# Kernel tuning notes

Measured on AMD Instinct MI355X. Metric: run time of the kernel, lower is better.

## Reference

```python
import jax, jax.numpy as jnp
import numpy as np

B, L, D, H = 2, 4096, 768, 12
Dh = D // H


def setup_inputs() -> dict:
    key = jax.random.key(0)
    k1, k2, k3 = jax.random.split(key, 3)
    x = jax.random.normal(k1, (B, L, D), dtype=jnp.float32)
    Wqkv = jax.random.normal(k2, (D, 3 * D), dtype=jnp.float32) * 0.02
    bqkv = jnp.zeros((3 * D,), dtype=jnp.float32)
    Wo = jax.random.normal(k3, (D, D), dtype=jnp.float32) * 0.02
    bo = jnp.zeros((D,), dtype=jnp.float32)
    return {"x": x, "Wqkv": Wqkv, "bqkv": bqkv, "Wo": Wo, "bo": bo}


def reference(x, Wqkv, bqkv, Wo, bo):
    Bs, Ls, Ds = x.shape
    # fused QKV projection
    qkv = x @ Wqkv + bqkv  # [B, L, 3D]
    q, k, v = jnp.split(qkv, 3, axis=2)
    q = q.reshape(Bs, Ls, H, Dh)
    k = k.reshape(Bs, Ls, H, Dh)
    v = v.reshape(Bs, Ls, H, Dh)
    # scaled dot-product attention with causal mask (fp32 softmax, as flax dpa with dtype=float32)
    scale = 1.0 / np.sqrt(Dh)
    scores = jnp.einsum('bqhd,bkhd->bhqk', q, k) * scale  # [B, H, L, L]
    causal = jnp.tril(jnp.ones((Ls, Ls), dtype=bool))
    big_neg = jnp.finfo(jnp.float32).min
    scores = jnp.where(causal[None, None, :, :], scores, big_neg)
    attn = jax.nn.softmax(scores, axis=-1)
    y = jnp.einsum('bhqk,bkhd->bqhd', attn, v)  # [B, L, H, Dh]
    y = y.reshape(Bs, Ls, Ds)
    # output projection
    return y @ Wo + bo
```

## Files before the change

kernel.cpp:

```cpp
#include <hip/hip_runtime.h>
#include <hip/hip_bf16.h>
#include <stdint.h>

#define BB 2
#define LL 4096
#define DD 768
#define HH 12
#define DH 64
#define MM (BB * LL)
#define NQKV (3 * DD)
#define KK 768
#define PLANE ((size_t)BB * HH * LL * DH)
#define SQSCALE 0.1803368801111204f

typedef __attribute__((ext_vector_type(8))) short bf16x8;
typedef __attribute__((ext_vector_type(4))) float f32x4;

__device__ __forceinline__ float bf2f(uint16_t u) {
  union { uint32_t u; float f; } c; c.u = ((uint32_t)u) << 16; return c.f;
}
__device__ __forceinline__ uint16_t f2bf(float f) {
  union { float f; uint32_t u; } c; c.f = f;
  return (uint16_t)((c.u + 0x7FFFu + ((c.u >> 16) & 1u)) >> 16);
}
__device__ __forceinline__ uint32_t cvt2(float a, float b) {
  __hip_bfloat162 h = __float22bfloat162_rn(make_float2(a, b));
  union { __hip_bfloat162 h; uint32_t u; } c; c.h = h; return c.u;
}

union H8 { uint16_t h[8]; uint32_t w[4]; uint4 v; };
union B8 { uint2 d[2]; bf16x8 v; };

template <bool F32>
__device__ __forceinline__ H8 load8(const void* p, size_t idx) {
  H8 r;
  if (F32) {
    const float* f = (const float*)p + idx;
    float4 a = *(const float4*)f;
    float4 b = *(const float4*)(f + 4);
    r.w[0] = cvt2(a.x, a.y); r.w[1] = cvt2(a.z, a.w);
    r.w[2] = cvt2(b.x, b.y); r.w[3] = cvt2(b.z, b.w);
  } else {
    r.v = *(const uint4*)((const uint16_t*)p + idx);
  }
  return r;
}

__device__ __forceinline__ void g2l16(const uint16_t* g, uint16_t* l) {
  __builtin_amdgcn_global_load_lds((const __attribute__((address_space(1))) void*)g,
                                   (__attribute__((address_space(3))) void*)l,
                                   16, 0, 0);
}

__global__ void detect_k(const uint16_t* __restrict__ x, int* __restrict__ flag) {
  __shared__ int cnt;
  if (threadIdx.x == 0) cnt = 0;
  __syncthreads();
  int c = 0;
  for (int i = threadIdx.x; i < 4096; i += 256) {
    int e = (x[i] >> 7) & 0xFF;
    if (e == 0xFF || e > 133 || e < 100) c++;
  }
  atomicAdd(&cnt, c);
  __syncthreads();
  if (threadIdx.x == 0) *flag = (cnt > 512) ? 1 : 0;
}

__global__ __launch_bounds__(256) void prep_k(const void* __restrict__ x,
                                              uint16_t* __restrict__ xbf,
                                              const void* __restrict__ Wqkv,
                                              uint16_t* __restrict__ wqkvT,
                                              const void* __restrict__ Wo,
                                              uint16_t* __restrict__ woT,
                                              const int* __restrict__ flag) {
  __shared__ uint16_t Ts[64][65];
  const int fl = *flag;
  const int id = blockIdx.x;
  const int tid = threadIdx.x;
  if (id < 768) {
    size_t base = (size_t)id * 1024 + tid;
#pragma unroll
    for (int j = 0; j < 4; ++j) {
      size_t i = base + j * 256;
      H8 v = fl ? load8<true>(x, i * 8) : load8<false>(x, i * 8);
      *(uint4*)(xbf + i * 8) = v.v;
    }
    return;
  }
  const void* W;
  uint16_t* WT;
  int N, widx;
  if (id < 1200) { W = Wqkv; WT = wqkvT; N = NQKV; widx = id - 768; }
  else           { W = Wo;   WT = woT;   N = DD;   widx = id - 1200; }
  const int nb = N / 64;
  const int n0 = (widx % nb) * 64, k0 = (widx / nb) * 64;
#pragma unroll
  for (int j = 0; j < 16; ++j) {
    int idx = tid + j * 256;
    int r = idx >> 6, c = idx & 63;
    size_t gi = (size_t)(k0 + r) * N + n0 + c;
    float v = fl ? ((const float*)W)[gi] : bf2f(((const uint16_t*)W)[gi]);
    Ts[c][r] = f2bf(v);
  }
  __syncthreads();
#pragma unroll
  for (int j = 0; j < 16; ++j) {
    int idx = tid + j * 256;
    int n = idx >> 6, k = idx & 63;
    WT[(size_t)(n0 + n) * KK + k0 + k] = Ts[n][k];
  }
}

__device__ __forceinline__ void gemm128_core(const uint16_t* __restrict__ A,
                                             const uint16_t* __restrict__ BT,
                                             int m0, int n0,
                                             uint16_t* As, uint16_t* Bs,
                                             f32x4 acc[4][4]) {
  const int tid = threadIdx.x, lane = tid & 63, w = tid >> 6;
  const int quad = lane >> 4, c16 = lane & 15;
  const int wm = w >> 1, wn = w & 1;
  const int srow = lane >> 2, schunk = lane & 3;
  const int rsw = (c16 >> 1) & 3;
  for (int k0 = 0; k0 < KK; k0 += 32) {
#pragma unroll
    for (int i = 0; i < 2; ++i) {
      int row = w * 32 + i * 16 + srow;
      int gch = schunk ^ ((row >> 1) & 3);
      g2l16(A + (size_t)(m0 + row) * KK + k0 + gch * 8, As + (w * 32 + i * 16) * 32);
      g2l16(BT + (size_t)(n0 + row) * KK + k0 + gch * 8, Bs + (w * 32 + i * 16) * 32);
    }
    __syncthreads();
    bf16x8 a[4], b[4];
#pragma unroll
    for (int i = 0; i < 4; ++i) {
      a[i] = *(const bf16x8*)(As + (wm * 64 + i * 16 + c16) * 32 + ((quad ^ rsw) * 8));
      b[i] = *(const bf16x8*)(Bs + (wn * 64 + i * 16 + c16) * 32 + ((quad ^ rsw) * 8));
    }
#pragma unroll
    for (int i = 0; i < 4; ++i)
#pragma unroll
      for (int f = 0; f < 4; ++f)
        acc[i][f] = __builtin_amdgcn_mfma_f32_16x16x32_bf16(a[i], b[f], acc[i][f], 0, 0, 0);
    __syncthreads();
  }
}

__global__ __launch_bounds__(256) void qkv128_k(const uint16_t* __restrict__ X,
                                                const uint16_t* __restrict__ WT,
                                                const void* __restrict__ bias,
                                                uint16_t* __restrict__ planes,
                                                const int* __restrict__ flag) {
  __shared__ __align__(16) uint16_t smem[8704];
  uint16_t* As = smem;
  uint16_t* Bs = smem + 4096;
  const int fl = *flag;
  const int m0 = blockIdx.x * 128, n0 = blockIdx.y * 128;
  f32x4 acc[4][4];
#pragma unroll
  for (int i = 0; i < 4; ++i)
#pragma unroll
    for (int f = 0; f < 4; ++f) acc[i][f] = (f32x4){0.f, 0.f, 0.f, 0.f};
  gemm128_core(X, WT, m0, n0, As, Bs, acc);

  const int tid = threadIdx.x, lane = tid & 63, w = tid >> 6;
  const int quad = lane >> 4, c16 = lane & 15;
  const int wm = w >> 1, wn = w & 1;
  const int which = (n0 >= 2 * DD) ? 2 : (n0 >= DD ? 1 : 0);

  if (which < 2) {
    uint16_t* dst = planes + (size_t)which * PLANE;
    const float sc = (which == 0) ? SQSCALE : 1.0f;
#pragma unroll
    for (int f = 0; f < 4; ++f) {
      int n = n0 + wn * 64 + f * 16 + c16;
      float bv = fl ? ((const float*)bias)[n] : bf2f(((const uint16_t*)bias)[n]);
      int rem = n - which * DD;
      int hh = rem >> 6, dd = rem & 63;
#pragma unroll
      for (int i = 0; i < 4; ++i) {
        uint32_t pa = cvt2((acc[i][f][0] + bv) * sc, (acc[i][f][1] + bv) * sc);
        uint32_t pb = cvt2((acc[i][f][2] + bv) * sc, (acc[i][f][3] + bv) * sc);
        int m = m0 + wm * 64 + i * 16 + quad * 4;
        int b = m >> 12, l = m & (LL - 1);
        uint16_t* base = dst + ((size_t)(b * HH + hh) * LL + l) * DH + dd;
        base[0 * DH] = (uint16_t)pa;
        base[1 * DH] = (uint16_t)(pa >> 16);
        base[2 * DH] = (uint16_t)pb;
        base[3 * DH] = (uint16_t)(pb >> 16);
      }
    }
  } else {
    uint16_t (*Ts)[136] = reinterpret_cast<uint16_t(*)[136]>(smem);
    uint16_t* vtp = planes + 2 * PLANE;
    const int l0 = m0 & (LL - 1), bb = m0 >> 12;
    for (int half = 0; half < 2; ++half) {
      __syncthreads();
      if (wn == half) {
#pragma unroll
        for (int f = 0; f < 4; ++f) {
          int n = n0 + half * 64 + f * 16 + c16;
          float bv = fl ? ((const float*)bias)[n] : bf2f(((const uint16_t*)bias)[n]);
#pragma unroll
          for (int i = 0; i < 4; ++i) {
            uint32_t pa = cvt2(acc[i][f][0] + bv, acc[i][f][1] + bv);
            uint32_t pb = cvt2(acc[i][f][2] + bv, acc[i][f][3] + bv);
            *(uint2*)(&Ts[f * 16 + c16][wm * 64 + i * 16 + quad * 4]) = make_uint2(pa, pb);
          }
        }
      }
      __syncthreads();
#pragma unroll
      for (int j = 0; j < 4; ++j) {
        int idx = tid + j * 256;
        int nl = idx >> 4, ch = idx & 15;
        int rem = n0 + half * 64 + nl - 2 * DD;
        int hh = rem >> 6, dd = rem & 63;
        uint4 val = *(const uint4*)(&Ts[nl][ch * 8]);
        *(uint4*)(vtp + ((size_t)(bb * HH + hh) * DH + dd) * LL + l0 + ch * 8) = val;
      }
    }
  }
}

__global__ __launch_bounds__(256) void attn_k(const uint16_t* __restrict__ planes,
                                              uint16_t* __restrict__ y) {
  __shared__ __align__(16) uint16_t Ks[2][64 * 64];
  __shared__ __align__(16) uint16_t Vt[2][64 * 64];
  __shared__ __align__(16) uint16_t Ps[4][16 * 64];
  const int p = blockIdx.x;
  const int bh = blockIdx.y;
  const uint16_t* qb = planes + (size_t)bh * LL * DH;
  const uint16_t* kb = qb + PLANE;
  const uint16_t* vtb = planes + 2 * PLANE + (size_t)bh * DH * LL;
  const int tid = threadIdx.x, lane = tid & 63, wv = tid >> 6;
  const int quad = lane >> 4, c16 = lane & 15;
  const int r0 = tid >> 3, c0 = tid & 7;
  const int sw0 = r0 & 7;
  const int swf = c16 & 7;
  uint16_t* Psb = Ps[wv];
  const int b = bh / HH, hh = bh - b * HH;
  const int pwbase = c16 * 64;
  const int prd0 = pwbase + (((2 * quad) ^ c16) << 2);
  const int prd1 = pwbase + (((2 * quad + 1) ^ c16) << 2);
  const int prd2 = pwbase + (((8 + 2 * quad) ^ c16) << 2);
  const int prd3 = pwbase + (((8 + 2 * quad + 1) ^ c16) << 2);

  for (int pass = 0; pass < 2; ++pass) {
    const int qi = pass ? p : 63 - p;
    const int q0 = qi * 64;
    const size_t qoff = (size_t)(q0 + wv * 16 + c16) * DH;
    bf16x8 qf0 = *(const bf16x8*)(qb + qoff + quad * 8);
    bf16x8 qf1 = *(const bf16x8*)(qb + qoff + 32 + quad * 8);

    f32x4 o[4];
#pragma unroll
    for (int g = 0; g < 4; ++g) o[g] = (f32x4){0.f, 0.f, 0.f, 0.f};
    float l_i = 0.f;

    uint4 kr0 = *(const uint4*)(kb + (size_t)r0 * DH + c0 * 8);
    uint4 kr1 = *(const uint4*)(kb + (size_t)(r0 + 32) * DH + c0 * 8);
    uint4 vr0 = *(const uint4*)(vtb + (size_t)r0 * LL + c0 * 8);
    uint4 vr1 = *(const uint4*)(vtb + (size_t)(r0 + 32) * LL + c0 * 8);

    for (int t = 0; t <= qi; ++t) {
      uint16_t* kd = Ks[t & 1];
      uint16_t* vd = Vt[t & 1];
      *(uint4*)(kd + r0 * 64 + (c0 ^ sw0) * 8) = kr0;
      *(uint4*)(kd + (r0 + 32) * 64 + (c0 ^ sw0) * 8) = kr1;
      *(uint4*)(vd + r0 * 64 + (c0 ^ sw0) * 8) = vr0;
      *(uint4*)(vd + (r0 + 32) * 64 + (c0 ^ sw0) * 8) = vr1;
      if (t < qi) {
        int t64 = (t + 1) * 64;
        kr0 = *(const uint4*)(kb + (size_t)(t64 + r0) * DH + c0 * 8);
        kr1 = *(const uint4*)(kb + (size_t)(t64 + r0 + 32) * DH + c0 * 8);
        vr0 = *(const uint4*)(vtb + (size_t)r0 * LL + t64 + c0 * 8);
        vr1 = *(const uint4*)(vtb + (size_t)(r0 + 32) * LL + t64 + c0 * 8);
      }
      __syncthreads();

      f32x4 s[4];
#pragma unroll
      for (int f = 0; f < 4; ++f) {
        const uint16_t* krow = kd + (f * 16 + c16) * 64;
        bf16x8 k0f = *(const bf16x8*)(krow + ((quad ^ swf) * 8));
        bf16x8 k1f = *(const bf16x8*)(krow + (((quad + 4) ^ swf) * 8));
        f32x4 z = {0.f, 0.f, 0.f, 0.f};
        z = __builtin_amdgcn_mfma_f32_16x16x32_bf16(k0f, qf0, z, 0, 0, 0);
        z = __builtin_amdgcn_mfma_f32_16x16x32_bf16(k1f, qf1, z, 0, 0, 0);
        s[f] = z;
      }
      const int qg = q0 + wv * 16 + c16;
      if (t == qi) {
#pragma unroll
        for (int f = 0; f < 4; ++f) {
          int key0 = t * 64 + f * 16 + quad * 4;
#pragma unroll
          for (int r = 0; r < 4; ++r) {
            float pv = exp2f(s[f][r]);
            pv = (key0 + r <= qg) ? pv : 0.f;
            s[f][r] = pv;
            l_i += pv;
          }
        }
      } else {
#pragma unroll
        for (int f = 0; f < 4; ++f)
#pragma unroll
          for (int r = 0; r < 4; ++r) {
            float pv = exp2f(s[f][r]);
            s[f][r] = pv;
            l_i += pv;
          }
      }
#pragma unroll
      for (int f = 0; f < 4; ++f) {
        uint32_t w0 = cvt2(s[f][0], s[f][1]);
        uint32_t w1 = cvt2(s[f][2], s[f][3]);
        *(uint2*)(Psb + pwbase + (((f * 4 + quad) ^ c16) << 2)) = make_uint2(w0, w1);
      }
      __asm__ __volatile__("s_waitcnt lgkmcnt(0)" ::: "memory");
      B8 p0, p1;
      p0.d[0] = *(const uint2*)(Psb + prd0);
      p0.d[1] = *(const uint2*)(Psb + prd1);
      p1.d[0] = *(const uint2*)(Psb + prd2);
      p1.d[1] = *(const uint2*)(Psb + prd3);
#pragma unroll
      for (int g = 0; g < 4; ++g) {
        const uint16_t* vrow = vd + (g * 16 + c16) * 64;
        bf16x8 v0 = *(const bf16x8*)(vrow + ((quad ^ swf) * 8));
        bf16x8 v1 = *(const bf16x8*)(vrow + (((quad + 4) ^ swf) * 8));
        o[g] = __builtin_amdgcn_mfma_f32_16x16x32_bf16(p0.v, v0, o[g], 0, 0, 0);
        o[g] = __builtin_amdgcn_mfma_f32_16x16x32_bf16(p1.v, v1, o[g], 0, 0, 0);
      }
    }

    l_i += __shfl_xor(l_i, 16);
    l_i += __shfl_xor(l_i, 32);
    float inv[4];
#pragma unroll
    for (int r = 0; r < 4; ++r)
      inv[r] = 1.f / __shfl(l_i, (quad << 4) + quad * 4 + r);
#pragma unroll
    for (int g = 0; g < 4; ++g) {
      uint32_t pa = cvt2(o[g][0] * inv[0], o[g][1] * inv[1]);
      uint32_t pb = cvt2(o[g][2] * inv[2], o[g][3] * inv[3]);
      int l = q0 + wv * 16 + quad * 4;
      uint16_t* base = y + ((size_t)(b * LL + l)) * DD + hh * DH + g * 16 + c16;
      base[0 * DD] = (uint16_t)pa;
      base[1 * DD] = (uint16_t)(pa >> 16);
      base[2 * DD] = (uint16_t)pb;
      base[3 * DD] = (uint16_t)(pb >> 16);
    }
    __syncthreads();
  }
}

__global__ __launch_bounds__(256) void out64_k(const uint16_t* __restrict__ Y,
                                               const uint16_t* __restrict__ WT,
                                               const void* __restrict__ bias,
                                               void* __restrict__ out,
                                               const int* __restrict__ flag) {
  __shared__ __align__(16) uint16_t As[128 * 32];
  __shared__ __align__(16) uint16_t Bs[64 * 32];
  const int fl = *flag;
  const int m0 = blockIdx.x * 128, n0 = blockIdx.y * 64;
  const int tid = threadIdx.x, lane = tid & 63, w = tid >> 6;
  const int quad = lane >> 4, c16 = lane & 15;
  const int srow = lane >> 2, schunk = lane & 3;
  const int rsw = (c16 >> 1) & 3;
  f32x4 acc[2][4];
#pragma unroll
  for (int i = 0; i < 2; ++i)
#pragma unroll
    for (int f = 0; f < 4; ++f) acc[i][f] = (f32x4){0.f, 0.f, 0.f, 0.f};
  for (int k0 = 0; k0 < KK; k0 += 32) {
#pragma unroll
    for (int i = 0; i < 2; ++i) {
      int row = w * 32 + i * 16 + srow;
      int gch = schunk ^ ((row >> 1) & 3);
      g2l16(Y + (size_t)(m0 + row) * KK + k0 + gch * 8, As + (w * 32 + i * 16) * 32);
    }
    {
      int row = w * 16 + srow;
      int gch = schunk ^ ((row >> 1) & 3);
      g2l16(WT + (size_t)(n0 + row) * KK + k0 + gch * 8, Bs + (w * 16) * 32);
    }
    __syncthreads();
    bf16x8 a[2], bfr[4];
#pragma unroll
    for (int i = 0; i < 2; ++i)
      a[i] = *(const bf16x8*)(As + (w * 32 + i * 16 + c16) * 32 + ((quad ^ rsw) * 8));
#pragma unroll
    for (int f = 0; f < 4; ++f)
      bfr[f] = *(const bf16x8*)(Bs + (f * 16 + c16) * 32 + ((quad ^ rsw) * 8));
#pragma unroll
    for (int i = 0; i < 2; ++i)
#pragma unroll
      for (int f = 0; f < 4; ++f)
        acc[i][f] = __builtin_amdgcn_mfma_f32_16x16x32_bf16(a[i], bfr[f], acc[i][f], 0, 0, 0);
    __syncthreads();
  }
#pragma unroll
  for (int f = 0; f < 4; ++f) {
    int n = n0 + f * 16 + c16;
    float bv = fl ? ((const float*)bias)[n] : bf2f(((const uint16_t*)bias)[n]);
#pragma unroll
    for (int i = 0; i < 2; ++i) {
      int m = m0 + w * 32 + i * 16 + quad * 4;
      if (fl) {
        float* base = (float*)out + (size_t)m * DD + n;
#pragma unroll
        for (int r = 0; r < 4; ++r) base[r * DD] = acc[i][f][r] + bv;
      } else {
        uint32_t pa = cvt2(acc[i][f][0] + bv, acc[i][f][1] + bv);
        uint32_t pb = cvt2(acc[i][f][2] + bv, acc[i][f][3] + bv);
        uint16_t* base = (uint16_t*)out + (size_t)m * DD + n;
        base[0 * DD] = (uint16_t)pa;
        base[1 * DD] = (uint16_t)(pa >> 16);
        base[2 * DD] = (uint16_t)pb;
        base[3 * DD] = (uint16_t)(pb >> 16);
      }
    }
  }
}

extern "C" void kernel_launch(void* const* d_in, const int* in_sizes, int n_in,
                              void* d_out, int out_size, void* d_ws, size_t ws_size,
                              hipStream_t stream) {
  const void* x    = d_in[0];
  const void* Wqkv = d_in[1];
  const void* bqkv = d_in[2];
  const void* Wo   = d_in[3];
  const void* bo   = d_in[4];
  int* flagp = (int*)d_ws;
  uint16_t* planes = (uint16_t*)((char*)d_ws + 64);
  uint16_t* y_ws   = planes + 3 * PLANE;
  uint16_t* wqkvT  = y_ws + (size_t)MM * DD;
  uint16_t* woT    = wqkvT + (size_t)NQKV * KK;
  uint16_t* xbf    = y_ws;

  detect_k<<<1, 256, 0, stream>>>((const uint16_t*)x, flagp);
  prep_k<<<1344, 256, 0, stream>>>(x, xbf, Wqkv, wqkvT, Wo, woT, flagp);
  qkv128_k<<<dim3(MM / 128, NQKV / 128), 256, 0, stream>>>(xbf, wqkvT, bqkv, planes, flagp);
  attn_k<<<dim3(32, BB * HH), 256, 0, stream>>>(planes, y_ws);
  out64_k<<<dim3(MM / 128, DD / 64), 256, 0, stream>>>(y_ws, woT, bo, d_out, flagp);
}
```

Before: 269.3 us.

## Fuse both causal query tiles into one K/V sweep and skip bf16 input copy

The attention kernel used to sweep K/V twice per block, once for the high query tile and once for the low one. It now sweeps once, loading each K/V tile into shared memory a single time and computing both query tiles against it while t <= ql. This halves K/V global loads and barrier count per block, at the cost of more registers for the second accumulator set, which may reduce occupancy. Separately, when the input is already bf16, the QKV GEMM reads x directly and the prep kernel skips the copy into the workspace.

```diff
diff --git a/kernel.cpp b/kernel.cpp
--- a/kernel.cpp
+++ b/kernel.cpp
@@ -78,11 +78,12 @@
   const int id = blockIdx.x;
   const int tid = threadIdx.x;
   if (id < 768) {
+    if (!fl) return;
     size_t base = (size_t)id * 1024 + tid;
 #pragma unroll
     for (int j = 0; j < 4; ++j) {
       size_t i = base + j * 256;
-      H8 v = fl ? load8<true>(x, i * 8) : load8<false>(x, i * 8);
+      H8 v = load8<true>(x, i * 8);
       *(uint4*)(xbf + i * 8) = v.v;
     }
     return;
@@ -145,7 +146,8 @@
   }
 }
 
-__global__ __launch_bounds__(256) void qkv128_k(const uint16_t* __restrict__ X,
+__global__ __launch_bounds__(256) void qkv128_k(const void* __restrict__ xorig,
+                                                const uint16_t* __restrict__ xbf,
                                                 const uint16_t* __restrict__ WT,
                                                 const void* __restrict__ bias,
                                                 uint16_t* __restrict__ planes,
@@ -154,6 +156,7 @@
   uint16_t* As = smem;
   uint16_t* Bs = smem + 4096;
   const int fl = *flag;
+  const uint16_t* X = fl ? xbf : (const uint16_t*)xorig;
   const int m0 = blockIdx.x * 128, n0 = blockIdx.y * 128;
   f32x4 acc[4][4];
 #pragma unroll
@@ -245,61 +248,94 @@
   const int prd2 = pwbase + (((8 + 2 * quad) ^ c16) << 2);
   const int prd3 = pwbase + (((8 + 2 * quad + 1) ^ c16) << 2);
 
-  for (int pass = 0; pass < 2; ++pass) {
-    const int qi = pass ? p : 63 - p;
-    const int q0 = qi * 64;
-    const size_t qoff = (size_t)(q0 + wv * 16 + c16) * DH;
-    bf16x8 qf0 = *(const bf16x8*)(qb + qoff + quad * 8);
-    bf16x8 qf1 = *(const bf16x8*)(qb + qoff + 32 + quad * 8);
-
-    f32x4 o[4];
-#pragma unroll
-    for (int g = 0; g < 4; ++g) o[g] = (f32x4){0.f, 0.f, 0.f, 0.f};
-    float l_i = 0.f;
-
-    uint4 kr0 = *(const uint4*)(kb + (size_t)r0 * DH + c0 * 8);
-    uint4 kr1 = *(const uint4*)(kb + (size_t)(r0 + 32) * DH + c0 * 8);
-    uint4 vr0 = *(const uint4*)(vtb + (size_t)r0 * LL + c0 * 8);
-    uint4 vr1 = *(const uint4*)(vtb + (size_t)(r0 + 32) * LL + c0 * 8);
-
-    for (int t = 0; t <= qi; ++t) {
-      uint16_t* kd = Ks[t & 1];
-      uint16_t* vd = Vt[t & 1];
-      *(uint4*)(kd + r0 * 64 + (c0 ^ sw0) * 8) = kr0;
-      *(uint4*)(kd + (r0 + 32) * 64 + (c0 ^ sw0) * 8) = kr1;
-      *(uint4*)(vd + r0 * 64 + (c0 ^ sw0) * 8) = vr0;
-      *(uint4*)(vd + (r0 + 32) * 64 + (c0 ^ sw0) * 8) = vr1;
-      if (t < qi) {
-        int t64 = (t + 1) * 64;
-        kr0 = *(const uint4*)(kb + (size_t)(t64 + r0) * DH + c0 * 8);
-        kr1 = *(const uint4*)(kb + (size_t)(t64 + r0 + 32) * DH + c0 * 8);
-        vr0 = *(const uint4*)(vtb + (size_t)r0 * LL + t64 + c0 * 8);
-        vr1 = *(const uint4*)(vtb + (size_t)(r0 + 32) * LL + t64 + c0 * 8);
-      }
-      __syncthreads();
-
-      f32x4 s[4];
+  const int qh = 63 - p, ql = p;
+  const size_t qoh = (size_t)(qh * 64 + wv * 16 + c16) * DH;
+  const size_t qol = (size_t)(ql * 64 + wv * 16 + c16) * DH;
+  bf16x8 qh0 = *(const bf16x8*)(qb + qoh + quad * 8);
+  bf16x8 qh1 = *(const bf16x8*)(qb + qoh + 32 + quad * 8);
+  bf16x8 ql0 = *(const bf16x8*)(qb + qol + quad * 8);
+  bf16x8 ql1 = *(const bf16x8*)(qb + qol + 32 + quad * 8);
+
+  f32x4 oh[4], ol[4];
+#pragma unroll
+  for (int g = 0; g < 4; ++g) { oh[g] = (f32x4){0.f,0.f,0.f,0.f}; ol[g] = (f32x4){0.f,0.f,0.f,0.f}; }
+  float lh = 0.f, llo = 0.f;
+
+  uint4 kr0 = *(const uint4*)(kb + (size_t)r0 * DH + c0 * 8);
+  uint4 kr1 = *(const uint4*)(kb + (size_t)(r0 + 32) * DH + c0 * 8);
+  uint4 vr0 = *(const uint4*)(vtb + (size_t)r0 * LL + c0 * 8);
+  uint4 vr1 = *(const uint4*)(vtb + (size_t)(r0 + 32) * LL + c0 * 8);
+
+  const int qgh = qh * 64 + wv * 16 + c16;
+  const int qgl = ql * 64 + wv * 16 + c16;
+
+  for (int t = 0; t <= qh; ++t) {
+    uint16_t* kd = Ks[t & 1];
+    uint16_t* vd = Vt[t & 1];
+    *(uint4*)(kd + r0 * 64 + (c0 ^ sw0) * 8) = kr0;
+    *(uint4*)(kd + (r0 + 32) * 64 + (c0 ^ sw0) * 8) = kr1;
+    *(uint4*)(vd + r0 * 64 + (c0 ^ sw0) * 8) = vr0;
+    *(uint4*)(vd + (r0 + 32) * 64 + (c0 ^ sw0) * 8) = vr1;
+    if (t < qh) {
+      int t64 = (t + 1) * 64;
+      kr0 = *(const uint4*)(kb + (size_t)(t64 + r0) * DH + c0 * 8);
+      kr1 = *(const uint4*)(kb + (size_t)(t64 + r0 + 32) * DH + c0 * 8);
+      vr0 = *(const uint4*)(vtb + (size_t)r0 * LL + t64 + c0 * 8);
+      vr1 = *(const uint4*)(vtb + (size_t)(r0 + 32) * LL + t64 + c0 * 8);
+    }
+    __syncthreads();
+
+    const bool dolo = (t <= ql);
+    f32x4 sh[4], sl[4];
+#pragma unroll
+    for (int f = 0; f < 4; ++f) {
+      const uint16_t* krow = kd + (f * 16 + c16) * 64;
+      bf16x8 k0f = *(const bf16x8*)(krow + ((quad ^ swf) * 8));
+      bf16x8 k1f = *(const bf16x8*)(krow + (((quad + 4) ^ swf) * 8));
+      f32x4 z = {0.f, 0.f, 0.f, 0.f};
+      z = __builtin_amdgcn_mfma_f32_16x16x32_bf16(k0f, qh0, z, 0, 0, 0);
+      z = __builtin_amdgcn_mfma_f32_16x16x32_bf16(k1f, qh1, z, 0, 0, 0);
+      sh[f] = z;
+      if (dolo) {
+        f32x4 zl = {0.f, 0.f, 0.f, 0.f};
+        zl = __builtin_amdgcn_mfma_f32_16x16x32_bf16(k0f, ql0, zl, 0, 0, 0);
+        zl = __builtin_amdgcn_mfma_f32_16x16x32_bf16(k1f, ql1, zl, 0, 0, 0);
+        sl[f] = zl;
+      }
+    }
+    if (t == qh) {
 #pragma unroll
       for (int f = 0; f < 4; ++f) {
-        const uint16_t* krow = kd + (f * 16 + c16) * 64;
-        bf16x8 k0f = *(const bf16x8*)(krow + ((quad ^ swf) * 8));
-        bf16x8 k1f = *(const bf16x8*)(krow + (((quad + 4) ^ swf) * 8));
-        f32x4 z = {0.f, 0.f, 0.f, 0.f};
-        z = __builtin_amdgcn_mfma_f32_16x16x32_bf16(k0f, qf0, z, 0, 0, 0);
-        z = __builtin_amdgcn_mfma_f32_16x16x32_bf16(k1f, qf1, z, 0, 0, 0);
-        s[f] = z;
-      }
-      const int qg = q0 + wv * 16 + c16;
-      if (t == qi) {
+        int key0 = t * 64 + f * 16 + quad * 4;
+#pragma unroll
+        for (int r = 0; r < 4; ++r) {
+          float pv = exp2f(sh[f][r]);
+          pv = (key0 + r <= qgh) ? pv : 0.f;
+          sh[f][r] = pv;
+          lh += pv;
+        }
+      }
+    } else {
+#pragma unroll
+      for (int f = 0; f < 4; ++f)
+#pragma unroll
+        for (int r = 0; r < 4; ++r) {
+          float pv = exp2f(sh[f][r]);
+          sh[f][r] = pv;
+          lh += pv;
+        }
+    }
+    if (dolo) {
+      if (t == ql) {
 #pragma unroll
         for (int f = 0; f < 4; ++f) {
           int key0 = t * 64 + f * 16 + quad * 4;
 #pragma unroll
           for (int r = 0; r < 4; ++r) {
-            float pv = exp2f(s[f][r]);
-            pv = (key0 + r <= qg) ? pv : 0.f;
-            s[f][r] = pv;
-            l_i += pv;
+            float pv = exp2f(sl[f][r]);
+            pv = (key0 + r <= qgl) ? pv : 0.f;
+            sl[f][r] = pv;
+            llo += pv;
           }
         }
       } else {
@@ -307,33 +343,56 @@
         for (int f = 0; f < 4; ++f)
 #pragma unroll
           for (int r = 0; r < 4; ++r) {
-            float pv = exp2f(s[f][r]);
-            s[f][r] = pv;
-            l_i += pv;
+            float pv = exp2f(sl[f][r]);
+            sl[f][r] = pv;
+            llo += pv;
           }
       }
+    }
+#pragma unroll
+    for (int f = 0; f < 4; ++f) {
+      uint32_t w0 = cvt2(sh[f][0], sh[f][1]);
+      uint32_t w1 = cvt2(sh[f][2], sh[f][3]);
+      *(uint2*)(Psb + pwbase + (((f * 4 + quad) ^ c16) << 2)) = make_uint2(w0, w1);
+    }
+    __asm__ __volatile__("s_waitcnt lgkmcnt(0)" ::: "memory");
+    B8 ph0, ph1;
+    ph0.d[0] = *(const uint2*)(Psb + prd0);
+    ph0.d[1] = *(const uint2*)(Psb + prd1);
+    ph1.d[0] = *(const uint2*)(Psb + prd2);
+    ph1.d[1] = *(const uint2*)(Psb + prd3);
+    B8 pl0, pl1;
+    if (dolo) {
 #pragma unroll
       for (int f = 0; f < 4; ++f) {
-        uint32_t w0 = cvt2(s[f][0], s[f][1]);
-        uint32_t w1 = cvt2(s[f][2], s[f][3]);
+        uint32_t w0 = cvt2(sl[f][0], sl[f][1]);
+        uint32_t w1 = cvt2(sl[f][2], sl[f][3]);
         *(uint2*)(Psb + pwbase + (((f * 4 + quad) ^ c16) << 2)) = make_uint2(w0, w1);
       }
       __asm__ __volatile__("s_waitcnt lgkmcnt(0)" ::: "memory");
-      B8 p0, p1;
-      p0.d[0] = *(const uint2*)(Psb + prd0);
-      p0.d[1] = *(const uint2*)(Psb + prd1);
-      p1.d[0] = *(const uint2*)(Psb + prd2);
-      p1.d[1] = *(const uint2*)(Psb + prd3);
-#pragma unroll
-      for (int g = 0; g < 4; ++g) {
-        const uint16_t* vrow = vd + (g * 16 + c16) * 64;
-        bf16x8 v0 = *(const bf16x8*)(vrow + ((quad ^ swf) * 8));
-        bf16x8 v1 = *(const bf16x8*)(vrow + (((quad + 4) ^ swf) * 8));
-        o[g] = __builtin_amdgcn_mfma_f32_16x16x32_bf16(p0.v, v0, o[g], 0, 0, 0);
-        o[g] = __builtin_amdgcn_mfma_f32_16x16x32_bf16(p1.v, v1, o[g], 0, 0, 0);
-      }
-    }
-
+      pl0.d[0] = *(const uint2*)(Psb + prd0);
+      pl0.d[1] = *(const uint2*)(Psb + prd1);
+      pl1.d[0] = *(const uint2*)(Psb + prd2);
+      pl1.d[1] = *(const uint2*)(Psb + prd3);
+    }
+#pragma unroll
+    for (int g = 0; g < 4; ++g) {
+      const uint16_t* vrow = vd + (g * 16 + c16) * 64;
+      bf16x8 v0 = *(const bf16x8*)(vrow + ((quad ^ swf) * 8));
+      bf16x8 v1 = *(const bf16x8*)(vrow + (((quad + 4) ^ swf) * 8));
+      oh[g] = __builtin_amdgcn_mfma_f32_16x16x32_bf16(ph0.v, v0, oh[g], 0, 0, 0);
+      oh[g] = __builtin_amdgcn_mfma_f32_16x16x32_bf16(ph1.v, v1, oh[g], 0, 0, 0);
+      if (dolo) {
+        ol[g] = __builtin_amdgcn_mfma_f32_16x16x32_bf16(pl0.v, v0, ol[g], 0, 0, 0);
+        ol[g] = __builtin_amdgcn_mfma_f32_16x16x32_bf16(pl1.v, v1, ol[g], 0, 0, 0);
+      }
+    }
+  }
+
+#pragma unroll
+  for (int side = 0; side < 2; ++side) {
+    float l_i = side ? llo : lh;
+    const int q0 = (side ? ql : qh) * 64;
     l_i += __shfl_xor(l_i, 16);
     l_i += __shfl_xor(l_i, 32);
     float inv[4];
@@ -342,8 +401,9 @@
       inv[r] = 1.f / __shfl(l_i, (quad << 4) + quad * 4 + r);
 #pragma unroll
     for (int g = 0; g < 4; ++g) {
-      uint32_t pa = cvt2(o[g][0] * inv[0], o[g][1] * inv[1]);
-      uint32_t pb = cvt2(o[g][2] * inv[2], o[g][3] * inv[3]);
+      f32x4 og = side ? ol[g] : oh[g];
+      uint32_t pa = cvt2(og[0] * inv[0], og[1] * inv[1]);
+      uint32_t pb = cvt2(og[2] * inv[2], og[3] * inv[3]);
       int l = q0 + wv * 16 + quad * 4;
       uint16_t* base = y + ((size_t)(b * LL + l)) * DD + hh * DH + g * 16 + c16;
       base[0 * DD] = (uint16_t)pa;
@@ -351,7 +411,6 @@
       base[2 * DD] = (uint16_t)pb;
       base[3 * DD] = (uint16_t)(pb >> 16);
     }
-    __syncthreads();
   }
 }
 
@@ -441,7 +500,7 @@
 
   detect_k<<<1, 256, 0, stream>>>((const uint16_t*)x, flagp);
   prep_k<<<1344, 256, 0, stream>>>(x, xbf, Wqkv, wqkvT, Wo, woT, flagp);
-  qkv128_k<<<dim3(MM / 128, NQKV / 128), 256, 0, stream>>>(xbf, wqkvT, bqkv, planes, flagp);
+  qkv128_k<<<dim3(MM / 128, NQKV / 128), 256, 0, stream>>>(x, xbf, wqkvT, bqkv, planes, flagp);
   attn_k<<<dim3(32, BB * HH), 256, 0, stream>>>(planes, y_ws);
   out64_k<<<dim3(MM / 128, DD / 64), 256, 0, stream>>>(y_ws, woT, bo, d_out, flagp);
 }
```

Result: slower. 305.2 us (+13.4%).

## Double GEMM K-tile to 64 with 8-chunk swizzle and skip bf16 x copy

Applied to the files above, without the earlier changes.

The QKV and output-projection GEMMs now stage 64-wide K slices in LDS instead of 32. The XOR swizzle is widened to 8 chunks, which halves the number of loop iterations and barrier pairs per tile. Separately, when the input is already bf16, the prep kernel no longer copies x into a workspace buffer, and the QKV GEMM reads the original input directly. The cost is twice the LDS per block, which may lower occupancy.

```diff
diff --git a/kernel.cpp b/kernel.cpp
--- a/kernel.cpp
+++ b/kernel.cpp
@@ -78,11 +78,12 @@
   const int id = blockIdx.x;
   const int tid = threadIdx.x;
   if (id < 768) {
+    if (!fl) return;
     size_t base = (size_t)id * 1024 + tid;
 #pragma unroll
     for (int j = 0; j < 4; ++j) {
       size_t i = base + j * 256;
-      H8 v = fl ? load8<true>(x, i * 8) : load8<false>(x, i * 8);
+      H8 v = load8<true>(x, i * 8);
       *(uint4*)(xbf + i * 8) = v.v;
     }
     return;
@@ -119,41 +120,47 @@
   const int tid = threadIdx.x, lane = tid & 63, w = tid >> 6;
   const int quad = lane >> 4, c16 = lane & 15;
   const int wm = w >> 1, wn = w & 1;
-  const int srow = lane >> 2, schunk = lane & 3;
-  const int rsw = (c16 >> 1) & 3;
-  for (int k0 = 0; k0 < KK; k0 += 32) {
-#pragma unroll
-    for (int i = 0; i < 2; ++i) {
-      int row = w * 32 + i * 16 + srow;
-      int gch = schunk ^ ((row >> 1) & 3);
-      g2l16(A + (size_t)(m0 + row) * KK + k0 + gch * 8, As + (w * 32 + i * 16) * 32);
-      g2l16(BT + (size_t)(n0 + row) * KK + k0 + gch * 8, Bs + (w * 32 + i * 16) * 32);
+  const int srow = lane >> 3, schunk = lane & 7;
+  const int rsw = c16 & 7;
+  for (int k0 = 0; k0 < KK; k0 += 64) {
+#pragma unroll
+    for (int j = 0; j < 4; ++j) {
+      int row = w * 32 + j * 8 + srow;
+      int gch = schunk ^ (row & 7);
+      g2l16(A + (size_t)(m0 + row) * KK + k0 + gch * 8, As + (w * 32 + j * 8) * 64);
+      g2l16(BT + (size_t)(n0 + row) * KK + k0 + gch * 8, Bs + (w * 32 + j * 8) * 64);
     }
     __syncthreads();
-    bf16x8 a[4], b[4];
-#pragma unroll
-    for (int i = 0; i < 4; ++i) {
-      a[i] = *(const bf16x8*)(As + (wm * 64 + i * 16 + c16) * 32 + ((quad ^ rsw) * 8));
-      b[i] = *(const bf16x8*)(Bs + (wn * 64 + i * 16 + c16) * 32 + ((quad ^ rsw) * 8));
-    }
-#pragma unroll
-    for (int i = 0; i < 4; ++i)
-#pragma unroll
-      for (int f = 0; f < 4; ++f)
-        acc[i][f] = __builtin_amdgcn_mfma_f32_16x16x32_bf16(a[i], b[f], acc[i][f], 0, 0, 0);
+#pragma unroll
+    for (int h = 0; h < 2; ++h) {
+      bf16x8 a[4], b[4];
+      const int ch = ((h * 4 + quad) ^ rsw) * 8;
+#pragma unroll
+      for (int i = 0; i < 4; ++i) {
+        a[i] = *(const bf16x8*)(As + (wm * 64 + i * 16 + c16) * 64 + ch);
+        b[i] = *(const bf16x8*)(Bs + (wn * 64 + i * 16 + c16) * 64 + ch);
+      }
+#pragma unroll
+      for (int i = 0; i < 4; ++i)
+#pragma unroll
+        for (int f = 0; f < 4; ++f)
+          acc[i][f] = __builtin_amdgcn_mfma_f32_16x16x32_bf16(a[i], b[f], acc[i][f], 0, 0, 0);
+    }
     __syncthreads();
   }
 }
 
-__global__ __launch_bounds__(256) void qkv128_k(const uint16_t* __restrict__ X,
+__global__ __launch_bounds__(256) void qkv128_k(const void* __restrict__ xorig,
+                                                const uint16_t* __restrict__ xbf,
                                                 const uint16_t* __restrict__ WT,
                                                 const void* __restrict__ bias,
                                                 uint16_t* __restrict__ planes,
                                                 const int* __restrict__ flag) {
-  __shared__ __align__(16) uint16_t smem[8704];
+  __shared__ __align__(16) uint16_t smem[16384];
   uint16_t* As = smem;
-  uint16_t* Bs = smem + 4096;
+  uint16_t* Bs = smem + 8192;
   const int fl = *flag;
+  const uint16_t* X = fl ? xbf : (const uint16_t*)xorig;
   const int m0 = blockIdx.x * 128, n0 = blockIdx.y * 128;
   f32x4 acc[4][4];
 #pragma unroll
@@ -360,44 +367,49 @@
                                                const void* __restrict__ bias,
                                                void* __restrict__ out,
                                                const int* __restrict__ flag) {
-  __shared__ __align__(16) uint16_t As[128 * 32];
-  __shared__ __align__(16) uint16_t Bs[64 * 32];
+  __shared__ __align__(16) uint16_t As[128 * 64];
+  __shared__ __align__(16) uint16_t Bs[64 * 64];
   const int fl = *flag;
   const int m0 = blockIdx.x * 128, n0 = blockIdx.y * 64;
   const int tid = threadIdx.x, lane = tid & 63, w = tid >> 6;
   const int quad = lane >> 4, c16 = lane & 15;
-  const int srow = lane >> 2, schunk = lane & 3;
-  const int rsw = (c16 >> 1) & 3;
+  const int srow = lane >> 3, schunk = lane & 7;
+  const int rsw = c16 & 7;
   f32x4 acc[2][4];
 #pragma unroll
   for (int i = 0; i < 2; ++i)
 #pragma unroll
     for (int f = 0; f < 4; ++f) acc[i][f] = (f32x4){0.f, 0.f, 0.f, 0.f};
-  for (int k0 = 0; k0 < KK; k0 += 32) {
-#pragma unroll
-    for (int i = 0; i < 2; ++i) {
-      int row = w * 32 + i * 16 + srow;
-      int gch = schunk ^ ((row >> 1) & 3);
-      g2l16(Y + (size_t)(m0 + row) * KK + k0 + gch * 8, As + (w * 32 + i * 16) * 32);
-    }
-    {
-      int row = w * 16 + srow;
-      int gch = schunk ^ ((row >> 1) & 3);
-      g2l16(WT + (size_t)(n0 + row) * KK + k0 + gch * 8, Bs + (w * 16) * 32);
+  for (int k0 = 0; k0 < KK; k0 += 64) {
+#pragma unroll
+    for (int j = 0; j < 4; ++j) {
+      int row = w * 32 + j * 8 + srow;
+      int gch = schunk ^ (row & 7);
+      g2l16(Y + (size_t)(m0 + row) * KK + k0 + gch * 8, As + (w * 32 + j * 8) * 64);
+    }
+#pragma unroll
+    for (int j = 0; j < 2; ++j) {
+      int row = w * 16 + j * 8 + srow;
+      int gch = schunk ^ (row & 7);
+      g2l16(WT + (size_t)(n0 + row) * KK + k0 + gch * 8, Bs + (w * 16 + j * 8) * 64);
     }
     __syncthreads();
-    bf16x8 a[2], bfr[4];
-#pragma unroll
-    for (int i = 0; i < 2; ++i)
-      a[i] = *(const bf16x8*)(As + (w * 32 + i * 16 + c16) * 32 + ((quad ^ rsw) * 8));
-#pragma unroll
-    for (int f = 0; f < 4; ++f)
-      bfr[f] = *(const bf16x8*)(Bs + (f * 16 + c16) * 32 + ((quad ^ rsw) * 8));
-#pragma unroll
-    for (int i = 0; i < 2; ++i)
+#pragma unroll
+    for (int h = 0; h < 2; ++h) {
+      const int ch = ((h * 4 + quad) ^ rsw) * 8;
+      bf16x8 a[2], bfr[4];
+#pragma unroll
+      for (int i = 0; i < 2; ++i)
+        a[i] = *(const bf16x8*)(As + (w * 32 + i * 16 + c16) * 64 + ch);
 #pragma unroll
       for (int f = 0; f < 4; ++f)
-        acc[i][f] = __builtin_amdgcn_mfma_f32_16x16x32_bf16(a[i], bfr[f], acc[i][f], 0, 0, 0);
+        bfr[f] = *(const bf16x8*)(Bs + (f * 16 + c16) * 64 + ch);
+#pragma unroll
+      for (int i = 0; i < 2; ++i)
+#pragma unroll
+        for (int f = 0; f < 4; ++f)
+          acc[i][f] = __builtin_amdgcn_mfma_f32_16x16x32_bf16(a[i], bfr[f], acc[i][f], 0, 0, 0);
+    }
     __syncthreads();
   }
 #pragma unroll
@@ -441,7 +453,7 @@
 
   detect_k<<<1, 256, 0, stream>>>((const uint16_t*)x, flagp);
   prep_k<<<1344, 256, 0, stream>>>(x, xbf, Wqkv, wqkvT, Wo, woT, flagp);
-  qkv128_k<<<dim3(MM / 128, NQKV / 128), 256, 0, stream>>>(xbf, wqkvT, bqkv, planes, flagp);
+  qkv128_k<<<dim3(MM / 128, NQKV / 128), 256, 0, stream>>>(x, xbf, wqkvT, bqkv, planes, flagp);
   attn_k<<<dim3(32, BB * HH), 256, 0, stream>>>(planes, y_ws);
   out64_k<<<dim3(MM / 128, DD / 64), 256, 0, stream>>>(y_ws, woT, bo, d_out, flagp);
 }
```

Measured after the change: 285.5 us. 6.0% more time.
